# Kernel optimization log

Hardware: AMD Instinct MI355X
Metric: run time of the kernel (lower is better)

## Reference

```python
import jax, jax.numpy as jnp
import numpy as np

B, T, I, H, O = 8, 4096, 128, 256, 64
H2 = 2 * H  # bidirectional feature size


def _init(key, shape, scale):
    return (jax.random.uniform(key, shape, jnp.float32) * 2.0 - 1.0) * scale


def setup_inputs() -> dict:
    key = jax.random.key(0)
    ks = jax.random.split(key, 14)
    s = 1.0 / np.sqrt(H)  # torch GRU init scale
    return {
        "x": jax.random.normal(ks[0], (B, T, I), jnp.float32),
        # forward-direction GRU params (gate order: r, z, n)
        "w_ih_f": _init(ks[1], (3 * H, I), s),
        "w_hh_f": _init(ks[2], (3 * H, H), s),
        "b_ih_f": _init(ks[3], (3 * H,), s),
        "b_hh_f": _init(ks[4], (3 * H,), s),
        # backward-direction GRU params
        "w_ih_b": _init(ks[5], (3 * H, I), s),
        "w_hh_b": _init(ks[6], (3 * H, H), s),
        "b_ih_b": _init(ks[7], (3 * H,), s),
        "b_hh_b": _init(ks[8], (3 * H,), s),
        # attention params
        "w_att": jax.random.normal(ks[9], (H2, H2), jnp.float32) * (1.0 / np.sqrt(H2)),
        "v_att": jax.random.normal(ks[10], (H2, 1), jnp.float32) * (1.0 / np.sqrt(H2)),
        # output linear
        "w_lin": _init(ks[11], (O, H2), 1.0 / np.sqrt(H2)),
        "b_lin": _init(ks[12], (O,), 1.0 / np.sqrt(H2)),
    }


def _run_gru(x, w_ih, w_hh, b_ih, b_hh, reverse):
    # x: [B,T,I] -> outputs [B,T,H]. PyTorch GRU cell math, gates ordered r,z,n.
    gx = jnp.einsum("bti,gi->btg", x, w_ih) + b_ih  # precompute input gates [B,T,3H]
    gx = jnp.moveaxis(gx, 1, 0)  # [T,B,3H] for scan

    def step(h, gxt):
        gh = h @ w_hh.T + b_hh  # [B,3H]
        xr, xz, xn = jnp.split(gxt, 3, axis=-1)
        hr, hz, hn = jnp.split(gh, 3, axis=-1)
        r = jax.nn.sigmoid(xr + hr)
        z = jax.nn.sigmoid(xz + hz)
        n = jnp.tanh(xn + r * hn)
        h_new = (1.0 - z) * n + z * h
        return h_new, h_new

    h0 = jnp.zeros((x.shape[0], w_hh.shape[1]), x.dtype)
    _, hs = jax.lax.scan(step, h0, gx, reverse=reverse)  # outputs time-aligned
    return jnp.moveaxis(hs, 0, 1)  # [B,T,H]


def reference(x, w_ih_f, w_hh_f, b_ih_f, b_hh_f, w_ih_b, w_hh_b, b_ih_b, b_hh_b,
              w_att, v_att, w_lin, b_lin):
    hf = _run_gru(x, w_ih_f, w_hh_f, b_ih_f, b_hh_f, reverse=False)
    hb = _run_gru(x, w_ih_b, w_hh_b, b_ih_b, b_hh_b, reverse=True)
    pred = jnp.concatenate([hf, hb], axis=-1)  # [B,T,2H]
    # attention over time: fused replacement of per-timestep mm/cat loops
    squish = jnp.tanh(jnp.einsum("bth,hk->btk", pred, w_att))  # [B,T,2H]
    scores = jnp.einsum("btk,k->bt", squish, v_att[:, 0])  # [B,T]
    a = jax.nn.softmax(scores, axis=-1)  # [B,T]
    ctx = jnp.einsum("bt,bth->bh", a, pred)  # [B,2H]
    logits = ctx @ w_lin.T + b_lin  # [B,O]
    return jax.nn.softmax(logits, axis=-1)
```

## Files before the change

### kernel.cpp

```cpp
#include <hip/hip_runtime.h>
#include <cstdint>
#include <cstddef>

#define NB 8
#define NT 4096
#define NI 128
#define NH 256
#define NH2 512
#define NO 64
#define NSLICE 8
#define NJS 32

#define OFF_MIR   0
#define OFF_SC    16384
#define OFF_CTX   49152
#define OFF_WT    53248
#define OFF_PRED  315392
#define ZERO_FLOATS 53248

__global__ __launch_bounds__(384, 1) void gru_rec(
    const float* __restrict__ x,
    const float* __restrict__ w_ih_f, const float* __restrict__ w_hh_f,
    const float* __restrict__ b_ih_f, const float* __restrict__ b_hh_f,
    const float* __restrict__ w_ih_b, const float* __restrict__ w_hh_b,
    const float* __restrict__ b_ih_b, const float* __restrict__ b_hh_b,
    unsigned long long* __restrict__ mir, float* __restrict__ pred)
{
    const int wg = blockIdx.x;
    const int dir = wg & 1;
    const int bb = (wg >> 1) & 7;
    const int slice = wg >> 4;
    const int tid = threadIdx.x;
    const int row = tid >> 2;
    const int q = tid & 3;
    const int g = row >> 5;
    const int jj = row & 31;
    const int grow = g * NH + slice * NJS + jj;

    const float* wih = dir ? w_ih_b : w_ih_f;
    const float* whh = dir ? w_hh_b : w_hh_f;
    const float* bih = dir ? b_ih_b : b_ih_f;
    const float* bhh = dir ? b_hh_b : b_hh_f;

    float wh[64], wi[32];
    {
        const float* p = whh + (size_t)grow * NH + q * 64;
        #pragma unroll
        for (int i = 0; i < 16; ++i) {
            float4 v = *(const float4*)(p + i * 4);
            wh[4*i] = v.x; wh[4*i+1] = v.y; wh[4*i+2] = v.z; wh[4*i+3] = v.w;
        }
        const float* p2 = wih + (size_t)grow * NI + q * 32;
        #pragma unroll
        for (int i = 0; i < 8; ++i) {
            float4 v = *(const float4*)(p2 + i * 4);
            wi[4*i] = v.x; wi[4*i+1] = v.y; wi[4*i+2] = v.z; wi[4*i+3] = v.w;
        }
    }
    const float bi = bih[grow];
    const float bh = bhh[grow];

    __shared__ float h_lds[268];
    __shared__ float x_lds[140];
    __shared__ float gx_l[2][96], gh_l[2][96];

    unsigned long long* mb = mir + (size_t)(dir * NB + bb) * 2 * NH;
    const float* xb = x + (size_t)bb * NT * NI;
    float* predb = pred + (size_t)bb * NT * NH2 + dir * NH;

    if (tid < NH) h_lds[tid + 4 * (tid >> 6)] = 0.f;
    float hprev = 0.f;
    float xr0 = 0.f, xr1 = 0.f;
    if (tid >= 320) {
        const int i0 = tid - 320;
        const int t0 = dir ? (NT - 1) : 0;
        x_lds[i0 + 4 * (i0 >> 5)] = xb[(size_t)t0 * NI + i0];
        { const int c1 = i0 + 64; x_lds[c1 + 4 * (c1 >> 5)] = xb[(size_t)t0 * NI + c1]; }
        const int t1 = dir ? (NT - 2) : 1;
        xr0 = xb[(size_t)t1 * NI + i0];
        xr1 = xb[(size_t)t1 * NI + i0 + 64];
    }
    __syncthreads();

    {
        float ah0 = 0.f, ah1 = 0.f, ah2 = 0.f, ah3 = 0.f;
        float ax0 = 0.f, ax1 = 0.f;
        const float* hp = h_lds + q * 68;
        #pragma unroll
        for (int i = 0; i < 16; ++i) {
            ah0 += wh[i]      * hp[i];
            ah1 += wh[16 + i] * hp[16 + i];
            ah2 += wh[32 + i] * hp[32 + i];
            ah3 += wh[48 + i] * hp[48 + i];
        }
        const float* xp = x_lds + q * 36;
        #pragma unroll
        for (int i = 0; i < 16; ++i) {
            ax0 += wi[i]      * xp[i];
            ax1 += wi[16 + i] * xp[16 + i];
        }
        float ah = (ah0 + ah1) + (ah2 + ah3);
        float ax = ax0 + ax1;
        ah += __shfl_xor(ah, 1); ah += __shfl_xor(ah, 2);
        ax += __shfl_xor(ax, 1); ax += __shfl_xor(ax, 2);
        if (q == 0) { gx_l[0][row] = ax + bi; gh_l[0][row] = ah + bh; }
    }
    __syncthreads();

    for (int s = 0; s < NT; ++s) {
        const int t = dir ? (NT - 1 - s) : s;
        const int p = s & 1;
        const int pw = (s + 1) & 1;

        if (tid < NJS) {
            const float xr = gx_l[p][tid],      hr = gh_l[p][tid];
            const float xz = gx_l[p][32 + tid], hz = gh_l[p][32 + tid];
            const float xn = gx_l[p][64 + tid], hn = gh_l[p][64 + tid];
            const float r = 1.f / (1.f + __expf(-(xr + hr)));
            const float z = 1.f / (1.f + __expf(-(xz + hz)));
            const float y = xn + r * hn;
            const float e2 = __expf(-2.f * y);
            const float n = (1.f - e2) / (1.f + e2);
            const float hnew = (1.f - z) * n + z * hprev;
            const int c = slice * NJS + tid;
            const unsigned long long pk =
                ((unsigned long long)(unsigned)(s + 1) << 32) |
                (unsigned long long)__float_as_uint(hnew);
            __hip_atomic_store(mb + (size_t)pw * NH + c, pk,
                               __ATOMIC_RELAXED, __HIP_MEMORY_SCOPE_AGENT);
            predb[(size_t)t * NH2 + c] = hnew;
            h_lds[c + 4 * (c >> 6)] = hnew;
            hprev = hnew;
        } else if (tid >= 64 && tid < 288) {
            const int idx = tid - 64;
            const int rc = idx < slice * NJS ? idx : idx + NJS;
            const unsigned long long* ap = mb + (size_t)pw * NH + rc;
            const unsigned tag = (unsigned)(s + 1);
            unsigned long long pk;
            do {
                pk = __hip_atomic_load(ap, __ATOMIC_RELAXED,
                                       __HIP_MEMORY_SCOPE_AGENT);
            } while ((unsigned)(pk >> 32) != tag);
            h_lds[rc + 4 * (rc >> 6)] = __uint_as_float((unsigned)pk);
        } else if (tid >= 320) {
            const int i0 = tid - 320;
            x_lds[i0 + 4 * (i0 >> 5)] = xr0;
            { const int c1 = i0 + 64; x_lds[c1 + 4 * (c1 >> 5)] = xr1; }
            int tn = dir ? (NT - 3 - s) : (s + 2);
            tn = tn < 0 ? 0 : (tn >= NT ? NT - 1 : tn);
            xr0 = xb[(size_t)tn * NI + i0];
            xr1 = xb[(size_t)tn * NI + i0 + 64];
        }
        __syncthreads();

        if (s < NT - 1) {
            float ah0 = 0.f, ah1 = 0.f, ah2 = 0.f, ah3 = 0.f;
            float ax0 = 0.f, ax1 = 0.f;
            const float* hp = h_lds + q * 68;
            #pragma unroll
            for (int i = 0; i < 16; ++i) {
                ah0 += wh[i]      * hp[i];
                ah1 += wh[16 + i] * hp[16 + i];
                ah2 += wh[32 + i] * hp[32 + i];
                ah3 += wh[48 + i] * hp[48 + i];
            }
            const float* xp = x_lds + q * 36;
            #pragma unroll
            for (int i = 0; i < 16; ++i) {
                ax0 += wi[i]      * xp[i];
                ax1 += wi[16 + i] * xp[16 + i];
            }
            float ah = (ah0 + ah1) + (ah2 + ah3);
            float ax = ax0 + ax1;
            ah += __shfl_xor(ah, 1); ah += __shfl_xor(ah, 2);
            ax += __shfl_xor(ax, 1); ax += __shfl_xor(ax, 2);
            if (q == 0) { gx_l[pw][row] = ax + bi; gh_l[pw][row] = ah + bh; }
            __syncthreads();
        }
    }
}

__global__ void transpose_watt(const float* __restrict__ w_att, float* __restrict__ wT) {
    const int n = blockIdx.x * 256 + threadIdx.x;
    const int k = n >> 9, h = n & 511;
    wT[n] = w_att[h * NH2 + k];
}

__global__ __launch_bounds__(256) void scores_gemm(
    const float* __restrict__ pred, const float* __restrict__ wT,
    const float* __restrict__ v_att, float* __restrict__ scores)
{
    const int tt = blockIdx.x, kt = blockIdx.y, bb = blockIdx.z;
    const int tid = threadIdx.x;
    const int tx = tid & 15;
    const int ty = tid >> 4;
    __shared__ float As[64][68];
    __shared__ float Bs[64][68];
    __shared__ float red[64][17];
    float acc[4][4] = {{0.f}};
    const int t0 = tt * 64, k0 = kt * 64;
    const float* pb = pred + ((size_t)bb * NT + t0) * NH2;

    for (int hc = 0; hc < NH2; hc += 64) {
        #pragma unroll
        for (int r = 0; r < 4; ++r) {
            const int idx = tid + 256 * r;
            const int tr = idx >> 4;
            const int c4 = (idx & 15) * 4;
            float4 a = *(const float4*)(pb + (size_t)tr * NH2 + hc + c4);
            *(float4*)&As[tr][c4] = a;
            float4 w = *(const float4*)(wT + (size_t)(k0 + tr) * NH2 + hc + c4);
            Bs[c4 + 0][tr] = w.x; Bs[c4 + 1][tr] = w.y;
            Bs[c4 + 2][tr] = w.z; Bs[c4 + 3][tr] = w.w;
        }
        __syncthreads();
        #pragma unroll
        for (int h = 0; h < 64; ++h) {
            const float a0 = As[ty*4+0][h], a1 = As[ty*4+1][h];
            const float a2 = As[ty*4+2][h], a3 = As[ty*4+3][h];
            const float4 bv = *(const float4*)&Bs[h][tx*4];
            acc[0][0] += a0*bv.x; acc[0][1] += a0*bv.y; acc[0][2] += a0*bv.z; acc[0][3] += a0*bv.w;
            acc[1][0] += a1*bv.x; acc[1][1] += a1*bv.y; acc[1][2] += a1*bv.z; acc[1][3] += a1*bv.w;
            acc[2][0] += a2*bv.x; acc[2][1] += a2*bv.y; acc[2][2] += a2*bv.z; acc[2][3] += a2*bv.w;
            acc[3][0] += a3*bv.x; acc[3][1] += a3*bv.y; acc[3][2] += a3*bv.z; acc[3][3] += a3*bv.w;
        }
        __syncthreads();
    }
    const float4 vv = *(const float4*)(v_att + k0 + tx * 4);
    #pragma unroll
    for (int i = 0; i < 4; ++i) {
        const float p = tanhf(acc[i][0]) * vv.x + tanhf(acc[i][1]) * vv.y
                      + tanhf(acc[i][2]) * vv.z + tanhf(acc[i][3]) * vv.w;
        red[ty*4+i][tx] = p;
    }
    __syncthreads();
    if (tid < 64) {
        float ssum = 0.f;
        #pragma unroll
        for (int xx = 0; xx < 16; ++xx) ssum += red[tid][xx];
        atomicAdd(&scores[bb * NT + t0 + tid], ssum);
    }
}

__global__ void softmax_t(float* __restrict__ scores) {
    const int bb = blockIdx.x;
    const int tid = threadIdx.x;
    __shared__ float red[256];
    float m = -1e30f;
    for (int t = tid; t < NT; t += 256) m = fmaxf(m, scores[bb*NT + t]);
    red[tid] = m; __syncthreads();
    for (int s2 = 128; s2; s2 >>= 1) { if (tid < s2) red[tid] = fmaxf(red[tid], red[tid+s2]); __syncthreads(); }
    m = red[0]; __syncthreads();
    float sum = 0.f;
    for (int t = tid; t < NT; t += 256) sum += expf(scores[bb*NT + t] - m);
    red[tid] = sum; __syncthreads();
    for (int s2 = 128; s2; s2 >>= 1) { if (tid < s2) red[tid] += red[tid+s2]; __syncthreads(); }
    const float inv = 1.f / red[0];
    for (int t = tid; t < NT; t += 256) scores[bb*NT + t] = expf(scores[bb*NT + t] - m) * inv;
}

__global__ void ctx_kernel(const float* __restrict__ pred, const float* __restrict__ a,
                           float* __restrict__ ctx) {
    const int bb = blockIdx.x, ch = blockIdx.y;
    const int tid = threadIdx.x;
    const int t0 = ch * 128;
    float acc0 = 0.f, acc1 = 0.f;
    for (int t = 0; t < 128; ++t) {
        const float av = a[bb*NT + t0 + t];
        const float* p = pred + ((size_t)bb * NT + t0 + t) * NH2;
        acc0 += av * p[tid];
        acc1 += av * p[tid + 256];
    }
    atomicAdd(&ctx[bb*NH2 + tid], acc0);
    atomicAdd(&ctx[bb*NH2 + tid + 256], acc1);
}

__global__ __launch_bounds__(512) void final_kernel(
    const float* __restrict__ ctx, const float* __restrict__ w_lin,
    const float* __restrict__ b_lin, float* __restrict__ out)
{
    const int tid = threadIdx.x;
    const int bb = tid >> 6, o = tid & 63;
    __shared__ float cl[NB][NH2];
    for (int i = tid; i < NB * NH2; i += 512) cl[i >> 9][i & 511] = ctx[i];
    __syncthreads();
    float acc = b_lin[o];
    for (int h = 0; h < NH2; h += 4) {
        const float4 w = *(const float4*)&w_lin[o * NH2 + h];
        acc += cl[bb][h]*w.x + cl[bb][h+1]*w.y + cl[bb][h+2]*w.z + cl[bb][h+3]*w.w;
    }
    float m = acc;
    for (int off = 32; off; off >>= 1) m = fmaxf(m, __shfl_xor(m, off));
    const float e = expf(acc - m);
    float ssum = e;
    for (int off = 32; off; off >>= 1) ssum += __shfl_xor(ssum, off);
    out[tid] = e / ssum;
}

extern "C" void kernel_launch(void* const* d_in, const int* in_sizes, int n_in,
                              void* d_out, int out_size, void* d_ws, size_t ws_size,
                              hipStream_t stream) {
    (void)in_sizes; (void)n_in; (void)out_size; (void)ws_size;
    const float* x      = (const float*)d_in[0];
    const float* w_ih_f = (const float*)d_in[1];
    const float* w_hh_f = (const float*)d_in[2];
    const float* b_ih_f = (const float*)d_in[3];
    const float* b_hh_f = (const float*)d_in[4];
    const float* w_ih_b = (const float*)d_in[5];
    const float* w_hh_b = (const float*)d_in[6];
    const float* b_ih_b = (const float*)d_in[7];
    const float* b_hh_b = (const float*)d_in[8];
    const float* w_att  = (const float*)d_in[9];
    const float* v_att  = (const float*)d_in[10];
    const float* w_lin  = (const float*)d_in[11];
    const float* b_lin  = (const float*)d_in[12];

    float* ws     = (float*)d_ws;
    unsigned long long* mir = (unsigned long long*)(ws + OFF_MIR);
    float* scores = ws + OFF_SC;
    float* ctx    = ws + OFF_CTX;
    float* wT     = ws + OFF_WT;
    float* pred   = ws + OFF_PRED;
    float* out    = (float*)d_out;

    hipMemsetAsync(d_ws, 0, (size_t)ZERO_FLOATS * sizeof(float), stream);
    hipLaunchKernelGGL(transpose_watt, dim3(1024), dim3(256), 0, stream, w_att, wT);
    hipLaunchKernelGGL(gru_rec, dim3(128), dim3(384), 0, stream,
                       x, w_ih_f, w_hh_f, b_ih_f, b_hh_f,
                       w_ih_b, w_hh_b, b_ih_b, b_hh_b, mir, pred);
    hipLaunchKernelGGL(scores_gemm, dim3(64, 8, 8), dim3(256), 0, stream,
                       pred, wT, v_att, scores);
    hipLaunchKernelGGL(softmax_t, dim3(8), dim3(256), 0, stream, scores);
    hipLaunchKernelGGL(ctx_kernel, dim3(8, 32), dim3(256), 0, stream, pred, scores, ctx);
    hipLaunchKernelGGL(final_kernel, dim3(1), dim3(512), 0, stream, ctx, w_lin, b_lin, out);
}
```

Before: 5.236 ms.

## Move input-gate projection off the recurrent critical path into dedicated warps

The x·W_ih projection is taken out of the per-step matvec done by all 384 threads. It now runs one step ahead on idle lanes (threads 320–415, each holding a full 128-wide W_ih row), overlapping with the atomic polling phase. The r and z input gates are folded into gh_l, so the cell update reads pre-summed values. The block grows to 448 threads, with a new warp doing float4 x prefetching three steps ahead, and the spin-wait now issues loads in a pipelined way. This shortens the serial per-step path, at the cost of higher register use (wiF[128]) and extra threads.

```diff
diff --git a/kernel.cpp b/kernel.cpp
--- a/kernel.cpp
+++ b/kernel.cpp
@@ -10,6 +10,7 @@
 #define NO 64
 #define NSLICE 8
 #define NJS 32
+#define NTH 448
 
 #define OFF_MIR   0
 #define OFF_SC    16384
@@ -18,7 +19,7 @@
 #define OFF_PRED  315392
 #define ZERO_FLOATS 53248
 
-__global__ __launch_bounds__(384, 1) void gru_rec(
+__global__ __launch_bounds__(NTH, 1) void gru_rec(
     const float* __restrict__ x,
     const float* __restrict__ w_ih_f, const float* __restrict__ w_hh_f,
     const float* __restrict__ b_ih_f, const float* __restrict__ b_hh_f,
@@ -33,91 +34,90 @@
     const int tid = threadIdx.x;
     const int row = tid >> 2;
     const int q = tid & 3;
-    const int g = row >> 5;
-    const int jj = row & 31;
-    const int grow = g * NH + slice * NJS + jj;
 
     const float* wih = dir ? w_ih_b : w_ih_f;
     const float* whh = dir ? w_hh_b : w_hh_f;
     const float* bih = dir ? b_ih_b : b_ih_f;
     const float* bhh = dir ? b_hh_b : b_hh_f;
 
-    float wh[64], wi[32];
-    {
+    __shared__ float h_lds[268];
+    __shared__ __align__(16) float x_lds[2][128];
+    __shared__ float gx_l[2][96], gh_l[2][96];
+
+    float wh[64];
+    float bh = 0.f;
+    if (tid < 384) {
+        const int grow = (row >> 5) * NH + slice * NJS + (row & 31);
         const float* p = whh + (size_t)grow * NH + q * 64;
         #pragma unroll
         for (int i = 0; i < 16; ++i) {
             float4 v = *(const float4*)(p + i * 4);
             wh[4*i] = v.x; wh[4*i+1] = v.y; wh[4*i+2] = v.z; wh[4*i+3] = v.w;
         }
-        const float* p2 = wih + (size_t)grow * NI + q * 32;
-        #pragma unroll
-        for (int i = 0; i < 8; ++i) {
+        bh = bhh[grow];
+    }
+    float wiF[128];
+    float biX = 0.f;
+    const int rowX = tid - 320;
+    if (tid >= 320 && tid < 416) {
+        const int growX = (rowX >> 5) * NH + slice * NJS + (rowX & 31);
+        const float* p2 = wih + (size_t)growX * NI;
+        #pragma unroll
+        for (int i = 0; i < 32; ++i) {
             float4 v = *(const float4*)(p2 + i * 4);
-            wi[4*i] = v.x; wi[4*i+1] = v.y; wi[4*i+2] = v.z; wi[4*i+3] = v.w;
-        }
-    }
-    const float bi = bih[grow];
-    const float bh = bhh[grow];
-
-    __shared__ float h_lds[268];
-    __shared__ float x_lds[140];
-    __shared__ float gx_l[2][96], gh_l[2][96];
+            wiF[4*i] = v.x; wiF[4*i+1] = v.y; wiF[4*i+2] = v.z; wiF[4*i+3] = v.w;
+        }
+        biX = bih[growX];
+    }
 
     unsigned long long* mb = mir + (size_t)(dir * NB + bb) * 2 * NH;
     const float* xb = x + (size_t)bb * NT * NI;
     float* predb = pred + (size_t)bb * NT * NH2 + dir * NH;
 
-    if (tid < NH) h_lds[tid + 4 * (tid >> 6)] = 0.f;
+    for (int i = tid; i < 268; i += NTH) h_lds[i] = 0.f;
     float hprev = 0.f;
-    float xr0 = 0.f, xr1 = 0.f;
-    if (tid >= 320) {
-        const int i0 = tid - 320;
+    float4 xpre = make_float4(0.f, 0.f, 0.f, 0.f);
+    const int si0 = (tid - 416) * 4;
+    if (tid >= 416) {
         const int t0 = dir ? (NT - 1) : 0;
-        x_lds[i0 + 4 * (i0 >> 5)] = xb[(size_t)t0 * NI + i0];
-        { const int c1 = i0 + 64; x_lds[c1 + 4 * (c1 >> 5)] = xb[(size_t)t0 * NI + c1]; }
         const int t1 = dir ? (NT - 2) : 1;
-        xr0 = xb[(size_t)t1 * NI + i0];
-        xr1 = xb[(size_t)t1 * NI + i0 + 64];
-    }
-    __syncthreads();
-
-    {
-        float ah0 = 0.f, ah1 = 0.f, ah2 = 0.f, ah3 = 0.f;
-        float ax0 = 0.f, ax1 = 0.f;
-        const float* hp = h_lds + q * 68;
-        #pragma unroll
-        for (int i = 0; i < 16; ++i) {
-            ah0 += wh[i]      * hp[i];
-            ah1 += wh[16 + i] * hp[16 + i];
-            ah2 += wh[32 + i] * hp[32 + i];
-            ah3 += wh[48 + i] * hp[48 + i];
-        }
-        const float* xp = x_lds + q * 36;
-        #pragma unroll
-        for (int i = 0; i < 16; ++i) {
-            ax0 += wi[i]      * xp[i];
-            ax1 += wi[16 + i] * xp[16 + i];
-        }
-        float ah = (ah0 + ah1) + (ah2 + ah3);
-        float ax = ax0 + ax1;
-        ah += __shfl_xor(ah, 1); ah += __shfl_xor(ah, 2);
-        ax += __shfl_xor(ax, 1); ax += __shfl_xor(ax, 2);
-        if (q == 0) { gx_l[0][row] = ax + bi; gh_l[0][row] = ah + bh; }
+        const int t2 = dir ? (NT - 3) : 2;
+        *(float4*)&x_lds[0][si0] = *(const float4*)(xb + (size_t)t0 * NI + si0);
+        *(float4*)&x_lds[1][si0] = *(const float4*)(xb + (size_t)t1 * NI + si0);
+        xpre = *(const float4*)(xb + (size_t)t2 * NI + si0);
+    }
+    __syncthreads();
+    if (tid >= 320 && tid < 416) {
+        float a0 = 0.f, a1 = 0.f, a2 = 0.f, a3 = 0.f;
+        const float* xp = x_lds[0];
+        #pragma unroll
+        for (int i = 0; i < 32; ++i) {
+            a0 += wiF[i]      * xp[i];
+            a1 += wiF[32 + i] * xp[32 + i];
+            a2 += wiF[64 + i] * xp[64 + i];
+            a3 += wiF[96 + i] * xp[96 + i];
+        }
+        gx_l[0][rowX] = ((a0 + a1) + (a2 + a3)) + biX;
+    }
+    __syncthreads();
+    if (tid < 384 && q == 0) {
+        float v = bh;
+        if (row < 64) v += gx_l[0][row];
+        gh_l[0][row] = v;
     }
     __syncthreads();
 
     for (int s = 0; s < NT; ++s) {
         const int t = dir ? (NT - 1 - s) : s;
-        const int p = s & 1;
-        const int pw = (s + 1) & 1;
+        const int p = s & 1, pw = p ^ 1;
 
         if (tid < NJS) {
-            const float xr = gx_l[p][tid],      hr = gh_l[p][tid];
-            const float xz = gx_l[p][32 + tid], hz = gh_l[p][32 + tid];
-            const float xn = gx_l[p][64 + tid], hn = gh_l[p][64 + tid];
-            const float r = 1.f / (1.f + __expf(-(xr + hr)));
-            const float z = 1.f / (1.f + __expf(-(xz + hz)));
+            const float sr = gh_l[p][tid];
+            const float sz = gh_l[p][32 + tid];
+            const float xn = gx_l[p][64 + tid];
+            const float hn = gh_l[p][64 + tid];
+            const float r = 1.f / (1.f + __expf(-sr));
+            const float z = 1.f / (1.f + __expf(-sz));
             const float y = xn + r * hn;
             const float e2 = __expf(-2.f * y);
             const float n = (1.f - e2) / (1.f + e2);
@@ -132,49 +132,60 @@
             h_lds[c + 4 * (c >> 6)] = hnew;
             hprev = hnew;
         } else if (tid >= 64 && tid < 288) {
-            const int idx = tid - 64;
-            const int rc = idx < slice * NJS ? idx : idx + NJS;
-            const unsigned long long* ap = mb + (size_t)pw * NH + rc;
-            const unsigned tag = (unsigned)(s + 1);
-            unsigned long long pk;
-            do {
-                pk = __hip_atomic_load(ap, __ATOMIC_RELAXED,
-                                       __HIP_MEMORY_SCOPE_AGENT);
-            } while ((unsigned)(pk >> 32) != tag);
-            h_lds[rc + 4 * (rc >> 6)] = __uint_as_float((unsigned)pk);
+            if (s < NT - 1) {
+                const int idx = tid - 64;
+                const int rc = idx < slice * NJS ? idx : idx + NJS;
+                const unsigned long long* ap = mb + (size_t)pw * NH + rc;
+                const unsigned tag = (unsigned)(s + 1);
+                unsigned long long v0 = __hip_atomic_load(ap, __ATOMIC_RELAXED, __HIP_MEMORY_SCOPE_AGENT);
+                unsigned long long v1 = __hip_atomic_load(ap, __ATOMIC_RELAXED, __HIP_MEMORY_SCOPE_AGENT);
+                unsigned long long v2 = __hip_atomic_load(ap, __ATOMIC_RELAXED, __HIP_MEMORY_SCOPE_AGENT);
+                while ((unsigned)(v0 >> 32) != tag) {
+                    v0 = v1; v1 = v2;
+                    v2 = __hip_atomic_load(ap, __ATOMIC_RELAXED, __HIP_MEMORY_SCOPE_AGENT);
+                }
+                h_lds[rc + 4 * (rc >> 6)] = __uint_as_float((unsigned)v0);
+            }
+        } else if (tid >= 416) {
+            *(float4*)&x_lds[p][si0] = xpre;
+            int tn = dir ? (NT - 4 - s) : (s + 3);
+            tn = tn < 0 ? 0 : (tn >= NT ? NT - 1 : tn);
+            xpre = *(const float4*)(xb + (size_t)tn * NI + si0);
         } else if (tid >= 320) {
-            const int i0 = tid - 320;
-            x_lds[i0 + 4 * (i0 >> 5)] = xr0;
-            { const int c1 = i0 + 64; x_lds[c1 + 4 * (c1 >> 5)] = xr1; }
-            int tn = dir ? (NT - 3 - s) : (s + 2);
-            tn = tn < 0 ? 0 : (tn >= NT ? NT - 1 : tn);
-            xr0 = xb[(size_t)tn * NI + i0];
-            xr1 = xb[(size_t)tn * NI + i0 + 64];
+            if (s + 1 < NT) {
+                float a0 = 0.f, a1 = 0.f, a2 = 0.f, a3 = 0.f;
+                const float* xp = x_lds[pw];
+                #pragma unroll
+                for (int i = 0; i < 32; ++i) {
+                    a0 += wiF[i]      * xp[i];
+                    a1 += wiF[32 + i] * xp[32 + i];
+                    a2 += wiF[64 + i] * xp[64 + i];
+                    a3 += wiF[96 + i] * xp[96 + i];
+                }
+                gx_l[pw][rowX] = ((a0 + a1) + (a2 + a3)) + biX;
+            }
         }
         __syncthreads();
 
         if (s < NT - 1) {
-            float ah0 = 0.f, ah1 = 0.f, ah2 = 0.f, ah3 = 0.f;
-            float ax0 = 0.f, ax1 = 0.f;
-            const float* hp = h_lds + q * 68;
-            #pragma unroll
-            for (int i = 0; i < 16; ++i) {
-                ah0 += wh[i]      * hp[i];
-                ah1 += wh[16 + i] * hp[16 + i];
-                ah2 += wh[32 + i] * hp[32 + i];
-                ah3 += wh[48 + i] * hp[48 + i];
+            if (tid < 384) {
+                float ah0 = 0.f, ah1 = 0.f, ah2 = 0.f, ah3 = 0.f;
+                const float* hp = h_lds + q * 68;
+                #pragma unroll
+                for (int i = 0; i < 16; ++i) {
+                    ah0 += wh[i]      * hp[i];
+                    ah1 += wh[16 + i] * hp[16 + i];
+                    ah2 += wh[32 + i] * hp[32 + i];
+                    ah3 += wh[48 + i] * hp[48 + i];
+                }
+                float ah = (ah0 + ah1) + (ah2 + ah3);
+                ah += __shfl_xor(ah, 1); ah += __shfl_xor(ah, 2);
+                if (q == 0) {
+                    float v = ah + bh;
+                    if (row < 64) v += gx_l[pw][row];
+                    gh_l[pw][row] = v;
+                }
             }
-            const float* xp = x_lds + q * 36;
-            #pragma unroll
-            for (int i = 0; i < 16; ++i) {
-                ax0 += wi[i]      * xp[i];
-                ax1 += wi[16 + i] * xp[16 + i];
-            }
-            float ah = (ah0 + ah1) + (ah2 + ah3);
-            float ax = ax0 + ax1;
-            ah += __shfl_xor(ah, 1); ah += __shfl_xor(ah, 2);
-            ax += __shfl_xor(ax, 1); ax += __shfl_xor(ax, 2);
-            if (q == 0) { gx_l[pw][row] = ax + bi; gh_l[pw][row] = ah + bh; }
             __syncthreads();
         }
     }
@@ -325,7 +336,7 @@
 
     hipMemsetAsync(d_ws, 0, (size_t)ZERO_FLOATS * sizeof(float), stream);
     hipLaunchKernelGGL(transpose_watt, dim3(1024), dim3(256), 0, stream, w_att, wT);
-    hipLaunchKernelGGL(gru_rec, dim3(128), dim3(384), 0, stream,
+    hipLaunchKernelGGL(gru_rec, dim3(128), dim3(NTH), 0, stream,
                        x, w_ih_f, w_hh_f, b_ih_f, b_hh_f,
                        w_ih_b, w_hh_b, b_ih_b, b_hh_b, mir, pred);
     hipLaunchKernelGGL(scores_gemm, dim3(64, 8, 8), dim3(256), 0, stream,
```

Result: slower. 6.020 ms (+15.0%).
